# Kernel tuning notes

Measured on AMD Instinct MI355X. Metric: run time of the kernel, lower is better.

The kernel has to match this reference:

```python
import jax, jax.numpy as jnp
import numpy as np

B, W, F = 64, 128, 64          # batch, window (node feat dim), n_features (nodes)
H, OUTW = 4, 128               # num_heads, out window size
NEG_SLOPE = 0.2                # LeakyReLU negative slope (alpha)


def setup_inputs() -> dict:
    key = jax.random.key(0)
    ks = jax.random.split(key, 6)
    scale_in = 1.0 / np.sqrt(W)
    scale_a = 1.0 / np.sqrt(OUTW)
    return {
        "x": jax.random.normal(ks[0], (B, W, F), dtype=jnp.float32),
        "W_src": jax.random.normal(ks[1], (H * OUTW, W), dtype=jnp.float32) * scale_in,
        "b_src": jnp.zeros((H * OUTW,), dtype=jnp.float32),
        "W_dst": jax.random.normal(ks[2], (H * OUTW, W), dtype=jnp.float32) * scale_in,
        "b_dst": jnp.zeros((H * OUTW,), dtype=jnp.float32),
        "attn": jax.random.normal(ks[3], (H, OUTW), dtype=jnp.float32) * scale_a,
    }


def reference(x, W_src, b_src, W_dst, b_dst, attn):
    # x: [B, W, F] -> node features nf: [B, F, W] (F nodes, W-dim features)
    nf = jnp.transpose(x, (0, 2, 1))
    b, f, w = nf.shape
    h, outw = attn.shape
    # GATv2 separate source/destination projections (share_weights=False)
    fs = (nf @ W_src.T + b_src).reshape(b, f, h, outw)  # [B, F, H, outW]
    fd = (nf @ W_dst.T + b_dst).reshape(b, f, h, outw)
    # additive score over complete graph with self-loops: e[b,i,j,h,d]
    s = fs[:, :, None, :, :] + fd[:, None, :, :, :]      # [B, src, dst, H, outW]
    e = jnp.where(s >= 0, s, NEG_SLOPE * s)              # LeakyReLU
    scores = jnp.einsum('bijhd,hd->bhij', e, attn)       # [B, H, src, dst]
    # edge softmax: normalize over incoming edges (sources) per destination
    a = jax.nn.softmax(scores, axis=2)
    # weighted scatter-sum aggregation at destinations
    out = jnp.einsum('bhij,bihd->bjhd', a, fs)           # [B, F, H, outW]
    out = out.mean(axis=2)                               # mean over heads -> [B, F, outW]
    return jnp.transpose(out, (0, 2, 1))                 # [B, outW, F]
```

## Files before the change

### kernel.cpp

```cpp
#include <hip/hip_runtime.h>
#include <math.h>

#define BB 64
#define WW 128
#define FF 64
#define HH 4
#define OW 128


struct GemmRegion {
    float xq[64 * 64];
    float wq[2 * 128 * 68];
};
struct AttnRegion {
    float fsl[FF * 132];
    float fdl[FF * 132];
    float st[FF * 68];
    float A6[OW], B4[OW];
    float redm[16 * 64];
    float reds[16 * 64];
};
union SMem { GemmRegion g; AttnRegion a; };

__global__ __launch_bounds__(1024, 4) void gat_fused(
    const float* __restrict__ x,
    const float* __restrict__ Wsrc,
    const float* __restrict__ bsrc,
    const float* __restrict__ Wdst,
    const float* __restrict__ bdst,
    const float* __restrict__ attn,
    float* __restrict__ out)
{
    __shared__ __align__(16) SMem sm;
    __shared__ float bl[2 * 128];

    const int bx = blockIdx.x;
    const int h  = bx & 3;
    const int b  = bx >> 2;
    const int t  = threadIdx.x;

    const int m  = t >> 7;
    const int ig = (t >> 4) & 7;
    const int dg = t & 15;
    const int i0 = ig * 8;

    if (t < 256) bl[t] = (t & 128 ? bdst : bsrc)[h * 128 + (t & 127)];

    float acc[8][8] = {};

    for (int kh = 0; kh < 2; ++kh) {
        if (kh) __syncthreads();
        {
            const int k = t >> 4, iq = t & 15;
            *(float4*)&sm.g.xq[k * 64 + iq * 4] =
                *(const float4*)(x + ((size_t)b * WW + kh * 64 + k) * FF + iq * 4);
        }
        #pragma unroll
        for (int p = 0; p < 4; ++p) {
            const int idx = p * 1024 + t;
            const int mm = idx >> 11, d = (idx >> 4) & 127, q = idx & 15;
            *(float4*)&sm.g.wq[(mm * 128 + d) * 68 + q * 4] =
                *(const float4*)((mm ? Wdst : Wsrc)
                                 + (size_t)(h * 128 + d) * WW + kh * 64 + q * 4);
        }
        __syncthreads();

        if (t < 256) {
            #pragma unroll 2
            for (int k0 = 0; k0 < 64; k0 += 4) {
                float4 xv[8];
                #pragma unroll
                for (int kk = 0; kk < 4; ++kk) {
                    xv[kk * 2 + 0] = *(const float4*)&sm.g.xq[(k0 + kk) * 64 + i0];
                    xv[kk * 2 + 1] = *(const float4*)&sm.g.xq[(k0 + kk) * 64 + i0 + 4];
                }
                #pragma unroll
                for (int e = 0; e < 8; ++e) {
                    const float4 wv =
                        *(const float4*)&sm.g.wq[(m * 128 + dg + 16 * e) * 68 + k0];
                    #pragma unroll
                    for (int kk = 0; kk < 4; ++kk) {
                        const float wf = ((const float*)&wv)[kk];
                        const float* xa = (const float*)&xv[kk * 2];
                        const float* xb = (const float*)&xv[kk * 2 + 1];
                        acc[0][e] = fmaf(xa[0], wf, acc[0][e]);
                        acc[1][e] = fmaf(xa[1], wf, acc[1][e]);
                        acc[2][e] = fmaf(xa[2], wf, acc[2][e]);
                        acc[3][e] = fmaf(xa[3], wf, acc[3][e]);
                        acc[4][e] = fmaf(xb[0], wf, acc[4][e]);
                        acc[5][e] = fmaf(xb[1], wf, acc[5][e]);
                        acc[6][e] = fmaf(xb[2], wf, acc[6][e]);
                        acc[7][e] = fmaf(xb[3], wf, acc[7][e]);
                    }
                }
            }
        }
    }
    __syncthreads();

    if (t < 256) {
        float* dst = m ? sm.a.fdl : sm.a.fsl;
        #pragma unroll
        for (int e = 0; e < 8; ++e) {
            const int d = dg + 16 * e;
            const float bv = bl[m * 128 + d];
            #pragma unroll
            for (int ii = 0; ii < 8; ++ii)
                dst[(i0 + ii) * 132 + d] = acc[ii][e] + bv;
        }
    }
    if (t < 128) {
        const float av = attn[h * OW + t];
        sm.a.A6[t] = 0.6f * av;
        sm.a.B4[t] = 0.4f * av;
    }
    __syncthreads();

    if (t < 256) {
        const int i = t & 63, sel = t >> 6;
        const float* src = (sel < 2 ? sm.a.fsl : sm.a.fdl) + i * 132 + (sel & 1) * 64;
        const float* a6  = sm.a.A6 + (sel & 1) * 64;
        float s = 0.0f;
        #pragma unroll
        for (int c = 0; c < 16; ++c) {
            float4 fv = *(const float4*)&src[c * 4];
            float4 av = *(const float4*)&a6[c * 4];
            s = fmaf(fv.x, av.x, fmaf(fv.y, av.y, fmaf(fv.z, av.z, fmaf(fv.w, av.w, s))));
        }
        sm.a.redm[sel * 64 + i] = s;
    }
    __syncthreads();

    if (t < 512) {
        const int lane = t & 63;
        const int jl0  = (t >> 6) * 8;
        float sc[8] = {};
        #pragma unroll 4
        for (int c = 0; c < 32; ++c) {
            const int dd0 = c * 4;
            float4 fsv = *(const float4*)&sm.a.fsl[lane * 132 + dd0];
            float4 b4  = *(const float4*)&sm.a.B4[dd0];
            #pragma unroll
            for (int jj = 0; jj < 8; ++jj) {
                float4 fdv = *(const float4*)&sm.a.fdl[(jl0 + jj) * 132 + dd0];
                float r = sc[jj];
                r = fmaf(b4.x, fabsf(fsv.x + fdv.x), r);
                r = fmaf(b4.y, fabsf(fsv.y + fdv.y), r);
                r = fmaf(b4.z, fabsf(fsv.z + fdv.z), r);
                r = fmaf(b4.w, fabsf(fsv.w + fdv.w), r);
                sc[jj] = r;
            }
        }
        const float csl = sm.a.redm[lane] + sm.a.redm[64 + lane];
        float4 o0, o1;
        o0.x = sc[0] + csl + sm.a.redm[128 + jl0 + 0] + sm.a.redm[192 + jl0 + 0];
        o0.y = sc[1] + csl + sm.a.redm[128 + jl0 + 1] + sm.a.redm[192 + jl0 + 1];
        o0.z = sc[2] + csl + sm.a.redm[128 + jl0 + 2] + sm.a.redm[192 + jl0 + 2];
        o0.w = sc[3] + csl + sm.a.redm[128 + jl0 + 3] + sm.a.redm[192 + jl0 + 3];
        o1.x = sc[4] + csl + sm.a.redm[128 + jl0 + 4] + sm.a.redm[192 + jl0 + 4];
        o1.y = sc[5] + csl + sm.a.redm[128 + jl0 + 5] + sm.a.redm[192 + jl0 + 5];
        o1.z = sc[6] + csl + sm.a.redm[128 + jl0 + 6] + sm.a.redm[192 + jl0 + 6];
        o1.w = sc[7] + csl + sm.a.redm[128 + jl0 + 7] + sm.a.redm[192 + jl0 + 7];
        *(float4*)&sm.a.st[lane * 68 + jl0]     = o0;
        *(float4*)&sm.a.st[lane * 68 + jl0 + 4] = o1;
    }
    __syncthreads();

    {
        const int j = t & 63, s = t >> 6;
        const int i0s = s * 4;
        float mx = sm.a.st[i0s * 68 + j];
        #pragma unroll
        for (int k = 1; k < 4; ++k) mx = fmaxf(mx, sm.a.st[(i0s + k) * 68 + j]);
        sm.a.redm[s * 64 + j] = mx;
    }
    __syncthreads();
    {
        const int j = t & 63, s = t >> 6;
        const int i0s = s * 4;
        float mj = sm.a.redm[j];
        #pragma unroll
        for (int s2 = 1; s2 < 16; ++s2) mj = fmaxf(mj, sm.a.redm[s2 * 64 + j]);
        float ps = 0.0f;
        #pragma unroll
        for (int k = 0; k < 4; ++k) {
            float e = __expf(sm.a.st[(i0s + k) * 68 + j] - mj);
            sm.a.st[(i0s + k) * 68 + j] = e;
            ps += e;
        }
        sm.a.reds[s * 64 + j] = ps;
    }
    __syncthreads();

    if (t < 512) {
        const int j = t & 63, dblk = t >> 6;
        float l = 0.0f;
        #pragma unroll
        for (int s2 = 0; s2 < 16; ++s2) l += sm.a.reds[s2 * 64 + j];
        const float iv = 0.25f / l;

        float ag[16] = {};
        #pragma unroll 4
        for (int i = 0; i < FF; ++i) {
            const float p = sm.a.st[i * 68 + j];
            const float* fr = &sm.a.fsl[i * 132 + dblk * 16];
            float4 f0 = *(const float4*)(fr);
            float4 f1 = *(const float4*)(fr + 4);
            float4 f2 = *(const float4*)(fr + 8);
            float4 f3 = *(const float4*)(fr + 12);
            ag[0]  = fmaf(p, f0.x, ag[0]);  ag[1]  = fmaf(p, f0.y, ag[1]);
            ag[2]  = fmaf(p, f0.z, ag[2]);  ag[3]  = fmaf(p, f0.w, ag[3]);
            ag[4]  = fmaf(p, f1.x, ag[4]);  ag[5]  = fmaf(p, f1.y, ag[5]);
            ag[6]  = fmaf(p, f1.z, ag[6]);  ag[7]  = fmaf(p, f1.w, ag[7]);
            ag[8]  = fmaf(p, f2.x, ag[8]);  ag[9]  = fmaf(p, f2.y, ag[9]);
            ag[10] = fmaf(p, f2.z, ag[10]); ag[11] = fmaf(p, f2.w, ag[11]);
            ag[12] = fmaf(p, f3.x, ag[12]); ag[13] = fmaf(p, f3.y, ag[13]);
            ag[14] = fmaf(p, f3.z, ag[14]); ag[15] = fmaf(p, f3.w, ag[15]);
        }
        float* ob = out + ((size_t)b * OW + dblk * 16) * FF + j;
        #pragma unroll
        for (int e = 0; e < 16; ++e)
            atomicAdd(ob + e * FF, ag[e] * iv);
    }
}

extern "C" void kernel_launch(void* const* d_in, const int* in_sizes, int n_in,
                              void* d_out, int out_size, void* d_ws, size_t ws_size,
                              hipStream_t stream) {
    const float* x    = (const float*)d_in[0];
    const float* Wsrc = (const float*)d_in[1];
    const float* bsrc = (const float*)d_in[2];
    const float* Wdst = (const float*)d_in[3];
    const float* bdst = (const float*)d_in[4];
    const float* attn = (const float*)d_in[5];

    hipMemsetAsync(d_out, 0, (size_t)out_size, stream);
    gat_fused<<<BB * HH, 1024, 0, stream>>>(x, Wsrc, bsrc, Wdst, bdst, attn,
                                            (float*)d_out);
}
```

Before: 112.6 us.

## Shrink block to 512 threads, restructure GEMM inner loop, pad x tile

The block size drops from 1024 to 512 threads with a waves-per-EU attribute, and the staging loads and softmax reductions are reworked to cover rows with fewer threads. The GEMM inner loop now loads the eight weight vectors once per k-step and streams the x vectors, with unroll 1 to limit register pressure. The x tile row stride is padded to 68 to cut LDS bank conflicts. Half as many threads sit idle in the serial phases, but each remaining thread does more staging and reduction work.

```diff
diff --git a/kernel.cpp b/kernel.cpp
--- a/kernel.cpp
+++ b/kernel.cpp
@@ -9,7 +9,7 @@
 
 
 struct GemmRegion {
-    float xq[64 * 64];
+    float xq[64 * 68];
     float wq[2 * 128 * 68];
 };
 struct AttnRegion {
@@ -17,12 +17,14 @@
     float fdl[FF * 132];
     float st[FF * 68];
     float A6[OW], B4[OW];
-    float redm[16 * 64];
-    float reds[16 * 64];
+    float redm[8 * 64];
+    float reds[8 * 64];
 };
 union SMem { GemmRegion g; AttnRegion a; };
 
-__global__ __launch_bounds__(1024, 4) void gat_fused(
+__global__ void __launch_bounds__(512)
+__attribute__((amdgpu_waves_per_eu(2, 2)))
+gat_fused(
     const float* __restrict__ x,
     const float* __restrict__ Wsrc,
     const float* __restrict__ bsrc,
@@ -50,14 +52,16 @@
 
     for (int kh = 0; kh < 2; ++kh) {
         if (kh) __syncthreads();
-        {
-            const int k = t >> 4, iq = t & 15;
-            *(float4*)&sm.g.xq[k * 64 + iq * 4] =
+        #pragma unroll
+        for (int p = 0; p < 2; ++p) {
+            const int idx = p * 512 + t;
+            const int k = idx >> 4, iq = idx & 15;
+            *(float4*)&sm.g.xq[k * 68 + iq * 4] =
                 *(const float4*)(x + ((size_t)b * WW + kh * 64 + k) * FF + iq * 4);
         }
         #pragma unroll
-        for (int p = 0; p < 4; ++p) {
-            const int idx = p * 1024 + t;
+        for (int p = 0; p < 8; ++p) {
+            const int idx = p * 512 + t;
             const int mm = idx >> 11, d = (idx >> 4) & 127, q = idx & 15;
             *(float4*)&sm.g.wq[(mm * 128 + d) * 68 + q * 4] =
                 *(const float4*)((mm ? Wdst : Wsrc)
@@ -66,31 +70,27 @@
         __syncthreads();
 
         if (t < 256) {
-            #pragma unroll 2
+            #pragma unroll 1
             for (int k0 = 0; k0 < 64; k0 += 4) {
-                float4 xv[8];
+                float4 wv[8];
+                #pragma unroll
+                for (int e = 0; e < 8; ++e)
+                    wv[e] = *(const float4*)&sm.g.wq[(m * 128 + dg + 16 * e) * 68 + k0];
                 #pragma unroll
                 for (int kk = 0; kk < 4; ++kk) {
-                    xv[kk * 2 + 0] = *(const float4*)&sm.g.xq[(k0 + kk) * 64 + i0];
-                    xv[kk * 2 + 1] = *(const float4*)&sm.g.xq[(k0 + kk) * 64 + i0 + 4];
-                }
-                #pragma unroll
-                for (int e = 0; e < 8; ++e) {
-                    const float4 wv =
-                        *(const float4*)&sm.g.wq[(m * 128 + dg + 16 * e) * 68 + k0];
+                    const float4 xa = *(const float4*)&sm.g.xq[(k0 + kk) * 68 + i0];
+                    const float4 xb = *(const float4*)&sm.g.xq[(k0 + kk) * 68 + i0 + 4];
                     #pragma unroll
-                    for (int kk = 0; kk < 4; ++kk) {
-                        const float wf = ((const float*)&wv)[kk];
-                        const float* xa = (const float*)&xv[kk * 2];
-                        const float* xb = (const float*)&xv[kk * 2 + 1];
-                        acc[0][e] = fmaf(xa[0], wf, acc[0][e]);
-                        acc[1][e] = fmaf(xa[1], wf, acc[1][e]);
-                        acc[2][e] = fmaf(xa[2], wf, acc[2][e]);
-                        acc[3][e] = fmaf(xa[3], wf, acc[3][e]);
-                        acc[4][e] = fmaf(xb[0], wf, acc[4][e]);
-                        acc[5][e] = fmaf(xb[1], wf, acc[5][e]);
-                        acc[6][e] = fmaf(xb[2], wf, acc[6][e]);
-                        acc[7][e] = fmaf(xb[3], wf, acc[7][e]);
+                    for (int e = 0; e < 8; ++e) {
+                        const float wf = ((const float*)&wv[e])[kk];
+                        acc[0][e] = fmaf(xa.x, wf, acc[0][e]);
+                        acc[1][e] = fmaf(xa.y, wf, acc[1][e]);
+                        acc[2][e] = fmaf(xa.z, wf, acc[2][e]);
+                        acc[3][e] = fmaf(xa.w, wf, acc[3][e]);
+                        acc[4][e] = fmaf(xb.x, wf, acc[4][e]);
+                        acc[5][e] = fmaf(xb.y, wf, acc[5][e]);
+                        acc[6][e] = fmaf(xb.z, wf, acc[6][e]);
+                        acc[7][e] = fmaf(xb.w, wf, acc[7][e]);
                     }
                 }
             }
@@ -131,7 +131,7 @@
     }
     __syncthreads();
 
-    if (t < 512) {
+    {
         const int lane = t & 63;
         const int jl0  = (t >> 6) * 8;
         float sc[8] = {};
@@ -168,22 +168,22 @@
 
     {
         const int j = t & 63, s = t >> 6;
-        const int i0s = s * 4;
+        const int i0s = s * 8;
         float mx = sm.a.st[i0s * 68 + j];
         #pragma unroll
-        for (int k = 1; k < 4; ++k) mx = fmaxf(mx, sm.a.st[(i0s + k) * 68 + j]);
+        for (int k = 1; k < 8; ++k) mx = fmaxf(mx, sm.a.st[(i0s + k) * 68 + j]);
         sm.a.redm[s * 64 + j] = mx;
     }
     __syncthreads();
     {
         const int j = t & 63, s = t >> 6;
-        const int i0s = s * 4;
+        const int i0s = s * 8;
         float mj = sm.a.redm[j];
         #pragma unroll
-        for (int s2 = 1; s2 < 16; ++s2) mj = fmaxf(mj, sm.a.redm[s2 * 64 + j]);
+        for (int s2 = 1; s2 < 8; ++s2) mj = fmaxf(mj, sm.a.redm[s2 * 64 + j]);
         float ps = 0.0f;
         #pragma unroll
-        for (int k = 0; k < 4; ++k) {
+        for (int k = 0; k < 8; ++k) {
             float e = __expf(sm.a.st[(i0s + k) * 68 + j] - mj);
             sm.a.st[(i0s + k) * 68 + j] = e;
             ps += e;
@@ -192,11 +192,11 @@
     }
     __syncthreads();
 
-    if (t < 512) {
+    {
         const int j = t & 63, dblk = t >> 6;
         float l = 0.0f;
         #pragma unroll
-        for (int s2 = 0; s2 < 16; ++s2) l += sm.a.reds[s2 * 64 + j];
+        for (int s2 = 0; s2 < 8; ++s2) l += sm.a.reds[s2 * 64 + j];
         const float iv = 0.25f / l;
 
         float ag[16] = {};
@@ -235,6 +235,6 @@
     const float* attn = (const float*)d_in[5];
 
     hipMemsetAsync(d_out, 0, (size_t)out_size, stream);
-    gat_fused<<<BB * HH, 1024, 0, stream>>>(x, Wsrc, bsrc, Wdst, bdst, attn,
-                                            (float*)d_out);
+    gat_fused<<<BB * HH, 512, 0, stream>>>(x, Wsrc, bsrc, Wdst, bdst, attn,
+                                           (float*)d_out);
 }
```

Result: faster. 105.2 us (-6.6%).
